# Optimization experiments

Hardware: AMD Instinct MI355X
Metric: run time of the kernel (lower is better)

## Reference

```python
import jax, jax.numpy as jnp
import numpy as np

D_MODEL = 512
N_HEADS = 8
D_K = 64
D_V = 64
FACTOR = 1  # Autoformer AutoCorrelation default


def setup_inputs() -> dict:
    key = jax.random.key(0)
    ks = jax.random.split(key, 7)
    B, L = 8, 2048
    Q = jax.random.normal(ks[0], (B, L, D_MODEL), dtype=jnp.float32)
    K = jax.random.normal(ks[1], (B, L, D_MODEL), dtype=jnp.float32)
    V = jax.random.normal(ks[2], (B, L, D_MODEL), dtype=jnp.float32)
    s = 1.0 / np.sqrt(D_MODEL)
    WQ = jax.random.normal(ks[3], (D_MODEL, N_HEADS * D_K), dtype=jnp.float32) * s
    WK = jax.random.normal(ks[4], (D_MODEL, N_HEADS * D_K), dtype=jnp.float32) * s
    WV = jax.random.normal(ks[5], (D_MODEL, N_HEADS * D_V), dtype=jnp.float32) * s
    Wfc = jax.random.normal(ks[6], (N_HEADS * D_V, D_MODEL), dtype=jnp.float32) * s
    return {"Q": Q, "K": K, "V": V, "WQ": WQ, "WK": WK, "WV": WV, "Wfc": Wfc}


def _autocorrelation(q, k, v):
    # q, k, v: [B, L, H, E] (Autoformer AutoCorrelation, training-mode agg)
    B, L, H, E = q.shape
    qf = jnp.fft.rfft(q.transpose(0, 2, 3, 1), axis=-1)  # [B,H,E,Lf]
    kf = jnp.fft.rfft(k.transpose(0, 2, 3, 1), axis=-1)
    corr = jnp.fft.irfft(qf * jnp.conj(kf), n=L, axis=-1)  # [B,H,E,L]
    vals = v.transpose(0, 2, 3, 1)  # [B,H,E,L]
    top_k = int(FACTOR * np.log(L))
    mean_value = corr.mean(axis=(1, 2))  # [B,L] mean over heads & channels
    _, index = jax.lax.top_k(mean_value.mean(axis=0), top_k)  # [top_k] shared delays
    weights = mean_value[:, index]  # [B, top_k]
    tmp_corr = jax.nn.softmax(weights, axis=-1)  # [B, top_k]
    # roll(vals, -index[i]) along time for each selected delay, fully vectorized
    gather_idx = (jnp.arange(L)[None, :] + index[:, None]) % L  # [top_k, L]
    rolled = vals[..., gather_idx]  # [B,H,E,top_k,L]
    agg = jnp.einsum('bhekl,bk->bhel', rolled, tmp_corr)  # [B,H,E,L]
    return agg.transpose(0, 3, 1, 2)  # [B,L,H,E]


def reference(Q, K, V, WQ, WK, WV, Wfc):
    B, L, _ = Q.shape
    q_s = (Q @ WQ).reshape(B, L, N_HEADS, D_K)
    k_s = (K @ WK).reshape(B, L, N_HEADS, D_K)
    v_s = (V @ WV).reshape(B, L, N_HEADS, D_V)
    context = _autocorrelation(q_s, k_s, v_s)  # [B,L,H,Dv]
    context = context.reshape(B, L, N_HEADS * D_V)
    return context @ Wfc  # [B,L,d_model]
```

## Files before the change

### kernel.cpp

```cpp
#include <hip/hip_runtime.h>
#include <math.h>

#define B_ 8
#define L_ 2048
#define D_ 512
#define LOG2L 11
#define TOPK 7
#define M_ (B_ * L_)

typedef __attribute__((ext_vector_type(8))) _Float16 half8;
typedef __attribute__((ext_vector_type(4))) _Float16 half4;
typedef __attribute__((ext_vector_type(4))) float f32x4;

__global__ __launch_bounds__(256) void convw_kernel(
    const float* __restrict__ W0, const float* __restrict__ W1,
    const float* __restrict__ W2, const float* __restrict__ W3,
    _Float16* __restrict__ T0, _Float16* __restrict__ T1,
    _Float16* __restrict__ T2, _Float16* __restrict__ T3)
{
  __shared__ float tile[64][65];
  const int t = (int)threadIdx.x;
  const int mat = (int)blockIdx.x >> 6;
  const int tb = (int)blockIdx.x & 63;
  const float* W = (mat == 0) ? W0 : (mat == 1) ? W1 : (mat == 2) ? W2 : W3;
  _Float16* Wt = (mat == 0) ? T0 : (mat == 1) ? T1 : (mat == 2) ? T2 : T3;
  const int k0 = (tb >> 3) * 64;
  const int n0 = (tb & 7) * 64;
#pragma unroll
  for (int i = 0; i < 4; ++i) {
    const int kl = (t >> 4) + i * 16;
    const float4 v = *reinterpret_cast<const float4*>(&W[(size_t)(k0 + kl) * D_ + n0 + (t & 15) * 4]);
    tile[kl][(t & 15) * 4 + 0] = v.x;
    tile[kl][(t & 15) * 4 + 1] = v.y;
    tile[kl][(t & 15) * 4 + 2] = v.z;
    tile[kl][(t & 15) * 4 + 3] = v.w;
  }
  __syncthreads();
  const int nl = t >> 2, q = t & 3;
  half8 h0, h1;
#pragma unroll
  for (int j = 0; j < 8; ++j) {
    h0[j] = (_Float16)tile[q * 16 + j][nl];
    h1[j] = (_Float16)tile[q * 16 + 8 + j][nl];
  }
  _Float16* dst = &Wt[(size_t)(n0 + nl) * D_ + k0 + q * 16];
  *reinterpret_cast<half8*>(dst) = h0;
  *reinterpret_cast<half8*>(dst + 8) = h1;
}

#define LDSTR 40

template <int INBF, int OUTMODE>
__global__ __launch_bounds__(256) void gemm_f16_kernel(
    const float* __restrict__ Af, const _Float16* __restrict__ Ah,
    const _Float16* __restrict__ Wt,
    float* __restrict__ Cf, _Float16* __restrict__ Ch)
{
  __shared__ __align__(16) char smem[128 * LDSTR * 2 * 2];
  _Float16* sA = (_Float16*)smem;
  _Float16* sB = sA + 128 * LDSTR;

  const int tid = (int)threadIdx.x;
  const int lane = tid & 63, wave = tid >> 6;
  const int wr = (wave >> 1) << 6, wc = (wave & 1) << 6;
  const int m0 = ((int)blockIdx.x >> 2) << 7;
  const int n0 = ((int)blockIdx.x & 3) << 7;

  const int srow = tid >> 1;
  const int sc0 = (tid & 1) << 4;

  f32x4 acc[4][4];
  const f32x4 zero = {0.f, 0.f, 0.f, 0.f};
#pragma unroll
  for (int i = 0; i < 4; ++i)
#pragma unroll
    for (int j = 0; j < 4; ++j) acc[i][j] = zero;

  const int fr = lane & 15;
  const int g8 = (lane >> 4) << 3;

  for (int k0 = 0; k0 < D_; k0 += 32) {
    half8 ha0, ha1, hb0, hb1;
    if constexpr (INBF == 0) {
      const float* ap = Af + (size_t)(m0 + srow) * D_ + k0 + sc0;
      float tmp[16];
#pragma unroll
      for (int j = 0; j < 4; ++j) {
        const float4 v = *reinterpret_cast<const float4*>(ap + j * 4);
        tmp[j * 4 + 0] = v.x; tmp[j * 4 + 1] = v.y;
        tmp[j * 4 + 2] = v.z; tmp[j * 4 + 3] = v.w;
      }
#pragma unroll
      for (int j = 0; j < 8; ++j) { ha0[j] = (_Float16)tmp[j]; ha1[j] = (_Float16)tmp[8 + j]; }
    } else {
      const _Float16* ap = Ah + (size_t)(m0 + srow) * D_ + k0 + sc0;
      ha0 = *reinterpret_cast<const half8*>(ap);
      ha1 = *reinterpret_cast<const half8*>(ap + 8);
    }
    {
      const _Float16* bp = Wt + (size_t)(n0 + srow) * D_ + k0 + sc0;
      hb0 = *reinterpret_cast<const half8*>(bp);
      hb1 = *reinterpret_cast<const half8*>(bp + 8);
    }

    __syncthreads();
    *reinterpret_cast<half8*>(&sA[srow * LDSTR + sc0]) = ha0;
    *reinterpret_cast<half8*>(&sA[srow * LDSTR + sc0 + 8]) = ha1;
    *reinterpret_cast<half8*>(&sB[srow * LDSTR + sc0]) = hb0;
    *reinterpret_cast<half8*>(&sB[srow * LDSTR + sc0 + 8]) = hb1;
    __syncthreads();

    half8 afr[4], bfr[4];
#pragma unroll
    for (int i = 0; i < 4; ++i) {
      afr[i] = *reinterpret_cast<const half8*>(&sA[(wr + i * 16 + fr) * LDSTR + g8]);
      bfr[i] = *reinterpret_cast<const half8*>(&sB[(wc + i * 16 + fr) * LDSTR + g8]);
    }
#pragma unroll
    for (int mi = 0; mi < 4; ++mi)
#pragma unroll
      for (int ni = 0; ni < 4; ++ni)
        acc[mi][ni] = __builtin_amdgcn_mfma_f32_16x16x32_f16(afr[mi], bfr[ni], acc[mi][ni], 0, 0, 0);
  }

  const int orow = (lane >> 4) << 2;
  const int ocol = lane & 15;
  if constexpr (OUTMODE == 0) {
#pragma unroll
    for (int mi = 0; mi < 4; ++mi)
#pragma unroll
      for (int ni = 0; ni < 4; ++ni)
#pragma unroll
        for (int r = 0; r < 4; ++r)
          Cf[(size_t)(m0 + wr + mi * 16 + orow + r) * D_ + n0 + wc + ni * 16 + ocol] = acc[mi][ni][r];
  } else if constexpr (OUTMODE == 2) {
#pragma unroll
    for (int mi = 0; mi < 4; ++mi)
#pragma unroll
      for (int ni = 0; ni < 4; ++ni)
#pragma unroll
        for (int r = 0; r < 4; ++r)
          Ch[(size_t)(m0 + wr + mi * 16 + orow + r) * D_ + n0 + wc + ni * 16 + ocol] = (_Float16)acc[mi][ni][r];
  } else {
#pragma unroll
    for (int ni = 0; ni < 4; ++ni) {
      const size_t nrow = (size_t)(n0 + wc + ni * 16 + ocol) * M_;
#pragma unroll
      for (int mi = 0; mi < 4; ++mi) {
        half4 hv;
        hv[0] = (_Float16)acc[mi][ni][0]; hv[1] = (_Float16)acc[mi][ni][1];
        hv[2] = (_Float16)acc[mi][ni][2]; hv[3] = (_Float16)acc[mi][ni][3];
        *reinterpret_cast<half4*>(&Ch[nrow + m0 + wr + mi * 16 + orow]) = hv;
      }
    }
  }
}

__device__ __forceinline__ int rev11(int x) {
  return (int)(__brev((unsigned)x) >> (32 - LOG2L));
}

#define DCHUNK 4
#define PADI(i) ((i) + ((i) >> 5))

#define BFLY(j0, j1, wr_, wi_) { \
  const float ar = xr[j0], ai = xi[j0], br = xr[j1], bi = xi[j1]; \
  xr[j0] = ar + br; xi[j0] = ai + bi; \
  const float tr = ar - br, ti = ai - bi; \
  xr[j1] = tr * (wr_) - ti * (wi_); \
  xi[j1] = tr * (wi_) + ti * (wr_); }

__global__ __launch_bounds__(256) void corr_fft_kernel(
    const _Float16* __restrict__ qT, const _Float16* __restrict__ kT,
    float* __restrict__ S)
{
  __shared__ float re[2112];
  __shared__ float im[2112];
  const int t = (int)threadIdx.x;
  const int blk = (int)blockIdx.x;
  const int b = blk >> 7;
  const int d0 = (blk & 127) * DCHUNK;
  const int u2 = t & 31, u3 = t & 3;

  float w2048r, w2048i, w256r, w256i, w32r, w32i;
  {
    float s_, c_;
    __sincosf(-6.283185307179586f * (float)t / 2048.f, &s_, &c_);
    w2048r = c_; w2048i = s_;
    __sincosf(-6.283185307179586f * (float)u2 / 256.f, &s_, &c_);
    w256r = c_; w256i = s_;
    __sincosf(-6.283185307179586f * (float)u3 / 32.f, &s_, &c_);
    w32r = c_; w32i = s_;
  }
  const float w1024r = w2048r * w2048r - w2048i * w2048i, w1024i = 2.f * w2048r * w2048i;
  const float w512r  = w1024r * w1024r - w1024i * w1024i, w512i  = 2.f * w1024r * w1024i;
  const float w128r  = w256r * w256r - w256i * w256i,     w128i  = 2.f * w256r * w256i;
  const float w64r   = w128r * w128r - w128i * w128i,     w64i   = 2.f * w128r * w128i;
  const float w16r   = w32r * w32r - w32i * w32i,         w16i   = 2.f * w32r * w32i;
  const float w8r    = w16r * w16r - w16i * w16i,         w8i    = 2.f * w16r * w16i;

  const float C_ = 0.70710678118654752f;
  const float W8R[4] = {1.f, C_, 0.f, -C_};
  const float W8I[4] = {0.f, -C_, -1.f, -C_};

  float pr[8] = {}, pi_[8] = {};

  for (int dc = 0; dc < DCHUNK; ++dc) {
    const int d = d0 + dc;
    const _Float16* qrow = qT + (size_t)d * M_ + (size_t)b * L_;
    const _Float16* krow = kT + (size_t)d * M_ + (size_t)b * L_;

    float xr[8], xi[8];
#pragma unroll
    for (int j = 0; j < 8; ++j) {
      xr[j] = (float)qrow[t + 256 * j];
      xi[j] = (float)krow[t + 256 * j];
    }

#pragma unroll
    for (int j = 0; j < 4; ++j) {
      const float wr_ = w2048r * W8R[j] - w2048i * W8I[j];
      const float wi_ = w2048r * W8I[j] + w2048i * W8R[j];
      BFLY(j, j + 4, wr_, wi_);
    }
#pragma unroll
    for (int base = 0; base < 8; base += 4) {
      BFLY(base + 0, base + 2, w1024r, w1024i);
      BFLY(base + 1, base + 3, w1024i, -w1024r);
    }
#pragma unroll
    for (int a = 0; a < 8; a += 2) BFLY(a, a + 1, w512r, w512i);

    __syncthreads();
#pragma unroll
    for (int j = 0; j < 8; ++j) {
      const int p = t + 256 * j;
      re[PADI(p)] = xr[j]; im[PADI(p)] = xi[j];
    }
    __syncthreads();
#pragma unroll
    for (int j = 0; j < 8; ++j) {
      const int p = ((t >> 5) << 8) + u2 + 32 * j;
      xr[j] = re[PADI(p)]; xi[j] = im[PADI(p)];
    }

#pragma unroll
    for (int j = 0; j < 4; ++j) {
      const float wr_ = w256r * W8R[j] - w256i * W8I[j];
      const float wi_ = w256r * W8I[j] + w256i * W8R[j];
      BFLY(j, j + 4, wr_, wi_);
    }
#pragma unroll
    for (int base = 0; base < 8; base += 4) {
      BFLY(base + 0, base + 2, w128r, w128i);
      BFLY(base + 1, base + 3, w128i, -w128r);
    }
#pragma unroll
    for (int a = 0; a < 8; a += 2) BFLY(a, a + 1, w64r, w64i);

    __syncthreads();
#pragma unroll
    for (int j = 0; j < 8; ++j) {
      const int p = ((t >> 5) << 8) + u2 + 32 * j;
      re[PADI(p)] = xr[j]; im[PADI(p)] = xi[j];
    }
    __syncthreads();
#pragma unroll
    for (int j = 0; j < 8; ++j) {
      const int p = ((t >> 2) << 5) + u3 + 4 * j;
      xr[j] = re[PADI(p)]; xi[j] = im[PADI(p)];
    }

#pragma unroll
    for (int j = 0; j < 4; ++j) {
      const float wr_ = w32r * W8R[j] - w32i * W8I[j];
      const float wi_ = w32r * W8I[j] + w32i * W8R[j];
      BFLY(j, j + 4, wr_, wi_);
    }
#pragma unroll
    for (int base = 0; base < 8; base += 4) {
      BFLY(base + 0, base + 2, w16r, w16i);
      BFLY(base + 1, base + 3, w16i, -w16r);
    }
#pragma unroll
    for (int a = 0; a < 8; a += 2) BFLY(a, a + 1, w8r, w8i);

    __syncthreads();
#pragma unroll
    for (int j = 0; j < 8; ++j) {
      const int p = ((t >> 2) << 5) + u3 + 4 * j;
      re[PADI(p)] = xr[j]; im[PADI(p)] = xi[j];
    }
    __syncthreads();
#pragma unroll
    for (int j = 0; j < 8; ++j) {
      const int p = 8 * t + j;
      xr[j] = re[PADI(p)]; xi[j] = im[PADI(p)];
    }

#pragma unroll
    for (int base = 0; base < 8; base += 4) {
      BFLY(base + 0, base + 2, 1.f, 0.f);
      BFLY(base + 1, base + 3, 0.f, -1.f);
    }
#pragma unroll
    for (int a = 0; a < 8; a += 2) BFLY(a, a + 1, 1.f, 0.f);

#pragma unroll
    for (int j = 0; j < 8; ++j) {
      const int p = 8 * t + j;
      re[PADI(p)] = xr[j]; im[PADI(p)] = xi[j];
    }
    __syncthreads();

#pragma unroll
    for (int i = 0; i < 8; ++i) {
      const int p = t + 256 * i;
      const int f = rev11(p);
      const int fm = (L_ - f) & (L_ - 1);
      const int pm = rev11(fm);
      const float Ar = re[PADI(p)],  Ai = im[PADI(p)];
      const float Br = re[PADI(pm)], Bi = -im[PADI(pm)];
      const float Qr = 0.5f * (Ar + Br), Qi = 0.5f * (Ai + Bi);
      const float Cr = 0.5f * (Ai - Bi), Ci = 0.5f * (Ar - Br);
      pr[i]  += Qr * Cr - Qi * Ci;
      pi_[i] += Qr * Ci + Qi * Cr;
    }
  }

#pragma unroll
  for (int i = 0; i < 8; ++i) {
    const int p = t + 256 * i;
    atomicAdd(&S[((size_t)b * L_ + p) * 2 + 0], pr[i]);
    atomicAdd(&S[((size_t)b * L_ + p) * 2 + 1], pi_[i]);
  }
}

__global__ __launch_bounds__(256) void ifft_kernel(
    const float* __restrict__ S, float* __restrict__ mv)
{
  __shared__ float re[L_];
  __shared__ float im[L_];
  const int b = blockIdx.x;
  for (int p = (int)threadIdx.x; p < L_; p += 256) {
    re[p] = S[((size_t)b * L_ + p) * 2 + 0];
    im[p] = S[((size_t)b * L_ + p) * 2 + 1];
  }
  __syncthreads();
  for (int s = 1; s <= LOG2L; ++s) {
    const int half = 1 << (s - 1);
    for (int j = (int)threadIdx.x; j < (L_ >> 1); j += 256) {
      const int pos = j & (half - 1);
      const int i0 = ((j >> (s - 1)) << s) + pos;
      const int i1 = i0 + half;
      const float ang = 3.14159265358979323846f * (float)pos / (float)half;
      float wi, wr;
      __sincosf(ang, &wi, &wr);
      const float br = re[i1], bi = im[i1];
      const float tr = br * wr - bi * wi;
      const float ti = br * wi + bi * wr;
      const float ar = re[i0], ai = im[i0];
      re[i0] = ar + tr; im[i0] = ai + ti;
      re[i1] = ar - tr; im[i1] = ai - ti;
    }
    __syncthreads();
  }
  const float scale = 1.0f / ((float)D_ * (float)L_);
  for (int l = (int)threadIdx.x; l < L_; l += 256)
    mv[(size_t)b * L_ + l] = re[l] * scale;
}

__global__ __launch_bounds__(1024) void topk_kernel(
    const float* __restrict__ mv, int* __restrict__ idx, float* __restrict__ wts)
{
  __shared__ float vals[L_];
  __shared__ float wm[16];
  __shared__ int wi[16];
  __shared__ int chosen[TOPK];
  const int t = (int)threadIdx.x;
  const int lane = t & 63, wv = t >> 6;
  float s0 = 0.f, s1 = 0.f;
#pragma unroll
  for (int b = 0; b < B_; ++b) {
    s0 += mv[(size_t)b * L_ + t];
    s1 += mv[(size_t)b * L_ + t + 1024];
  }
  vals[t] = s0; vals[t + 1024] = s1;
  __syncthreads();
  for (int kk = 0; kk < TOPK; ++kk) {
    float v0 = vals[t]; int i0 = t;
    const float v1 = vals[t + 1024];
    if (v1 > v0) { v0 = v1; i0 = t + 1024; }
#pragma unroll
    for (int off = 32; off; off >>= 1) {
      const float ov = __shfl_xor(v0, off, 64);
      const int oi = __shfl_xor(i0, off, 64);
      if (ov > v0 || (ov == v0 && oi < i0)) { v0 = ov; i0 = oi; }
    }
    if (lane == 0) { wm[wv] = v0; wi[wv] = i0; }
    __syncthreads();
    if (t == 0) {
      float m = wm[0]; int mi = wi[0];
      for (int i2 = 1; i2 < 16; ++i2)
        if (wm[i2] > m || (wm[i2] == m && wi[i2] < mi)) { m = wm[i2]; mi = wi[i2]; }
      chosen[kk] = mi; idx[kk] = mi; vals[mi] = -1e30f;
    }
    __syncthreads();
  }
  if (t < B_) {
    float w[TOPK];
    float mx = -1e30f;
#pragma unroll
    for (int kk = 0; kk < TOPK; ++kk) {
      w[kk] = mv[(size_t)t * L_ + chosen[kk]];
      mx = fmaxf(mx, w[kk]);
    }
    float sum = 0.f;
#pragma unroll
    for (int kk = 0; kk < TOPK; ++kk) { w[kk] = __expf(w[kk] - mx); sum += w[kk]; }
    const float inv = 1.0f / sum;
#pragma unroll
    for (int kk = 0; kk < TOPK; ++kk) wts[t * TOPK + kk] = w[kk] * inv;
  }
}

__global__ __launch_bounds__(128) void context_kernel(
    const _Float16* __restrict__ v, const int* __restrict__ idx,
    const float* __restrict__ wts, _Float16* __restrict__ ctx)
{
  const int bl = (int)blockIdx.x;
  const int b = bl >> LOG2L;
  const int l = bl & (L_ - 1);
  const int c = (int)threadIdx.x;
  float acc0 = 0.f, acc1 = 0.f, acc2 = 0.f, acc3 = 0.f;
#pragma unroll
  for (int kk = 0; kk < TOPK; ++kk) {
    const float w = wts[b * TOPK + kk];
    const int src = (l + idx[kk]) & (L_ - 1);
    const half4 x = *reinterpret_cast<const half4*>(v + ((size_t)(b << LOG2L) + src) * D_ + c * 4);
    acc0 = fmaf(w, (float)x[0], acc0);
    acc1 = fmaf(w, (float)x[1], acc1);
    acc2 = fmaf(w, (float)x[2], acc2);
    acc3 = fmaf(w, (float)x[3], acc3);
  }
  half4 o;
  o[0] = (_Float16)acc0; o[1] = (_Float16)acc1;
  o[2] = (_Float16)acc2; o[3] = (_Float16)acc3;
  *reinterpret_cast<half4*>(ctx + ((size_t)(b << LOG2L) + l) * D_ + c * 4) = o;
}

extern "C" void kernel_launch(void* const* d_in, const int* in_sizes, int n_in,
                              void* d_out, int out_size, void* d_ws, size_t ws_size,
                              hipStream_t stream)
{
  (void)in_sizes; (void)n_in; (void)out_size; (void)ws_size;
  const float* Q   = (const float*)d_in[0];
  const float* K   = (const float*)d_in[1];
  const float* V   = (const float*)d_in[2];
  const float* WQ  = (const float*)d_in[3];
  const float* WK  = (const float*)d_in[4];
  const float* WV  = (const float*)d_in[5];
  const float* Wfc = (const float*)d_in[6];
  float* out = (float*)d_out;

  char* ws = (char*)d_ws;
  const size_t sz_h   = (size_t)M_ * D_ * sizeof(_Float16);
  const size_t sz_w16 = (size_t)D_ * D_ * sizeof(_Float16);
  _Float16*  qT16  = (_Float16*)(ws);
  _Float16*  kT16  = (_Float16*)(ws + sz_h);
  _Float16*  vs16  = (_Float16*)(ws + 2 * sz_h);
  _Float16*  ctx16 = (_Float16*)(ws + 3 * sz_h);
  _Float16*  WQt   = (_Float16*)(ws + 4 * sz_h);
  _Float16*  WKt   = (_Float16*)(ws + 4 * sz_h + sz_w16);
  _Float16*  WVt   = (_Float16*)(ws + 4 * sz_h + 2 * sz_w16);
  _Float16*  Wfct  = (_Float16*)(ws + 4 * sz_h + 3 * sz_w16);
  float*     S     = (float*)(ws + 4 * sz_h + 4 * sz_w16);
  float*     mv    = (float*)((char*)S + (size_t)B_ * L_ * 2 * sizeof(float));
  int*       idx   = (int*)((char*)mv + (size_t)B_ * L_ * sizeof(float));
  float*     wts   = (float*)((char*)idx + 64);

  convw_kernel<<<256, 256, 0, stream>>>(WQ, WK, WV, Wfc, WQt, WKt, WVt, Wfct);

  gemm_f16_kernel<0, 3><<<512, 256, 0, stream>>>(Q, nullptr, WQt, nullptr, qT16);
  gemm_f16_kernel<0, 3><<<512, 256, 0, stream>>>(K, nullptr, WKt, nullptr, kT16);

  hipMemsetAsync(S, 0, (size_t)B_ * L_ * 2 * sizeof(float), stream);
  corr_fft_kernel<<<B_ * (D_ / DCHUNK), 256, 0, stream>>>(qT16, kT16, S);
  ifft_kernel<<<B_, 256, 0, stream>>>(S, mv);
  topk_kernel<<<1, 1024, 0, stream>>>(mv, idx, wts);

  gemm_f16_kernel<0, 2><<<512, 256, 0, stream>>>(V, nullptr, WVt, nullptr, vs16);
  context_kernel<<<B_ * L_, 128, 0, stream>>>(vs16, idx, wts, ctx16);
  gemm_f16_kernel<1, 0><<<512, 256, 0, stream>>>(nullptr, ctx16, Wfct, out, nullptr);
}
```

Before: 182.5 us.

## Batch QKV GEMMs, halve FFT chunk, use Hermitian symmetry, widen context loads

Merges the three Q/K/V projection GEMMs into one 1536-block launch, with the output mode chosen at runtime. Halves DCHUNK so the correlation FFT kernel launches twice as many blocks, adding a sync between chunks. Atomic accumulation now covers only the non-redundant half of the spectrum, and the inverse FFT rebuilds the rest from conjugate symmetry. The context kernel processes four rows per 256-thread block with half8 loads. The runtime output-mode branch and the smaller per-block FFT work may add overhead in exchange for fewer launches and less atomic traffic.

```diff
diff --git a/kernel.cpp b/kernel.cpp
--- a/kernel.cpp
+++ b/kernel.cpp
@@ -50,11 +50,12 @@
 
 #define LDSTR 40
 
-template <int INBF, int OUTMODE>
-__global__ __launch_bounds__(256) void gemm_f16_kernel(
+template <int INBF>
+__device__ __forceinline__ void gemm_body(
     const float* __restrict__ Af, const _Float16* __restrict__ Ah,
     const _Float16* __restrict__ Wt,
-    float* __restrict__ Cf, _Float16* __restrict__ Ch)
+    float* __restrict__ Cf, _Float16* __restrict__ Ch,
+    int outmode, int blk)
 {
   __shared__ __align__(16) char smem[128 * LDSTR * 2 * 2];
   _Float16* sA = (_Float16*)smem;
@@ -63,8 +64,8 @@
   const int tid = (int)threadIdx.x;
   const int lane = tid & 63, wave = tid >> 6;
   const int wr = (wave >> 1) << 6, wc = (wave & 1) << 6;
-  const int m0 = ((int)blockIdx.x >> 2) << 7;
-  const int n0 = ((int)blockIdx.x & 3) << 7;
+  const int m0 = (blk >> 2) << 7;
+  const int n0 = (blk & 3) << 7;
 
   const int srow = tid >> 1;
   const int sc0 = (tid & 1) << 4;
@@ -125,7 +126,7 @@
 
   const int orow = (lane >> 4) << 2;
   const int ocol = lane & 15;
-  if constexpr (OUTMODE == 0) {
+  if (outmode == 0) {
 #pragma unroll
     for (int mi = 0; mi < 4; ++mi)
 #pragma unroll
@@ -133,7 +134,7 @@
 #pragma unroll
         for (int r = 0; r < 4; ++r)
           Cf[(size_t)(m0 + wr + mi * 16 + orow + r) * D_ + n0 + wc + ni * 16 + ocol] = acc[mi][ni][r];
-  } else if constexpr (OUTMODE == 2) {
+  } else if (outmode == 2) {
 #pragma unroll
     for (int mi = 0; mi < 4; ++mi)
 #pragma unroll
@@ -156,11 +157,34 @@
   }
 }
 
+__global__ __launch_bounds__(256) void gemm_qkv_kernel(
+    const float* __restrict__ Q, const float* __restrict__ K,
+    const float* __restrict__ V,
+    const _Float16* __restrict__ WQt, const _Float16* __restrict__ WKt,
+    const _Float16* __restrict__ WVt,
+    _Float16* __restrict__ qT16, _Float16* __restrict__ kT16,
+    _Float16* __restrict__ vs16)
+{
+  const int mat = (int)blockIdx.x >> 9;
+  const int blk = (int)blockIdx.x & 511;
+  const float* A = (mat == 0) ? Q : (mat == 1) ? K : V;
+  const _Float16* Wt = (mat == 0) ? WQt : (mat == 1) ? WKt : WVt;
+  _Float16* Ch = (mat == 0) ? qT16 : (mat == 1) ? kT16 : vs16;
+  gemm_body<0>(A, nullptr, Wt, nullptr, Ch, (mat == 2) ? 2 : 3, blk);
+}
+
+__global__ __launch_bounds__(256) void gemm_fc_kernel(
+    const _Float16* __restrict__ ctx16, const _Float16* __restrict__ Wfct,
+    float* __restrict__ out)
+{
+  gemm_body<1>(nullptr, ctx16, Wfct, out, nullptr, 0, (int)blockIdx.x);
+}
+
 __device__ __forceinline__ int rev11(int x) {
   return (int)(__brev((unsigned)x) >> (32 - LOG2L));
 }
 
-#define DCHUNK 4
+#define DCHUNK 2
 #define PADI(i) ((i) + ((i) >> 5))
 
 #define BFLY(j0, j1, wr_, wi_) { \
@@ -178,8 +202,8 @@
   __shared__ float im[2112];
   const int t = (int)threadIdx.x;
   const int blk = (int)blockIdx.x;
-  const int b = blk >> 7;
-  const int d0 = (blk & 127) * DCHUNK;
+  const int b = blk >> 8;
+  const int d0 = (blk & 255) * DCHUNK;
   const int u2 = t & 31, u3 = t & 3;
 
   float w2048r, w2048i, w256r, w256i, w32r, w32i;
@@ -326,13 +350,17 @@
       pr[i]  += Qr * Cr - Qi * Ci;
       pi_[i] += Qr * Ci + Qi * Cr;
     }
+    if (dc + 1 < DCHUNK) __syncthreads();
   }
 
 #pragma unroll
   for (int i = 0; i < 8; ++i) {
     const int p = t + 256 * i;
-    atomicAdd(&S[((size_t)b * L_ + p) * 2 + 0], pr[i]);
-    atomicAdd(&S[((size_t)b * L_ + p) * 2 + 1], pi_[i]);
+    const int f = rev11(p);
+    if (f <= L_ / 2) {
+      atomicAdd(&S[((size_t)b * L_ + p) * 2 + 0], pr[i]);
+      atomicAdd(&S[((size_t)b * L_ + p) * 2 + 1], pi_[i]);
+    }
   }
 }
 
@@ -343,8 +371,17 @@
   __shared__ float im[L_];
   const int b = blockIdx.x;
   for (int p = (int)threadIdx.x; p < L_; p += 256) {
-    re[p] = S[((size_t)b * L_ + p) * 2 + 0];
-    im[p] = S[((size_t)b * L_ + p) * 2 + 1];
+    const int f = rev11(p);
+    float sr, si;
+    if (f <= L_ / 2) {
+      sr = S[((size_t)b * L_ + p) * 2 + 0];
+      si = S[((size_t)b * L_ + p) * 2 + 1];
+    } else {
+      const int pm = rev11(L_ - f);
+      sr = S[((size_t)b * L_ + pm) * 2 + 0];
+      si = -S[((size_t)b * L_ + pm) * 2 + 1];
+    }
+    re[p] = sr; im[p] = si;
   }
   __syncthreads();
   for (int s = 1; s <= LOG2L; ++s) {
@@ -424,29 +461,27 @@
   }
 }
 
-__global__ __launch_bounds__(128) void context_kernel(
+__global__ __launch_bounds__(256) void context_kernel(
     const _Float16* __restrict__ v, const int* __restrict__ idx,
     const float* __restrict__ wts, _Float16* __restrict__ ctx)
 {
-  const int bl = (int)blockIdx.x;
-  const int b = bl >> LOG2L;
-  const int l = bl & (L_ - 1);
-  const int c = (int)threadIdx.x;
-  float acc0 = 0.f, acc1 = 0.f, acc2 = 0.f, acc3 = 0.f;
+  const int blk = (int)blockIdx.x;
+  const int b = blk >> 9;
+  const int l = ((blk & 511) << 2) + ((int)threadIdx.x >> 6);
+  const int lane = (int)threadIdx.x & 63;
+  float acc[8] = {};
 #pragma unroll
   for (int kk = 0; kk < TOPK; ++kk) {
     const float w = wts[b * TOPK + kk];
     const int src = (l + idx[kk]) & (L_ - 1);
-    const half4 x = *reinterpret_cast<const half4*>(v + ((size_t)(b << LOG2L) + src) * D_ + c * 4);
-    acc0 = fmaf(w, (float)x[0], acc0);
-    acc1 = fmaf(w, (float)x[1], acc1);
-    acc2 = fmaf(w, (float)x[2], acc2);
-    acc3 = fmaf(w, (float)x[3], acc3);
-  }
-  half4 o;
-  o[0] = (_Float16)acc0; o[1] = (_Float16)acc1;
-  o[2] = (_Float16)acc2; o[3] = (_Float16)acc3;
-  *reinterpret_cast<half4*>(ctx + ((size_t)(b << LOG2L) + l) * D_ + c * 4) = o;
+    const half8 x = *reinterpret_cast<const half8*>(v + ((size_t)(b << LOG2L) + src) * D_ + lane * 8);
+#pragma unroll
+    for (int j = 0; j < 8; ++j) acc[j] = fmaf(w, (float)x[j], acc[j]);
+  }
+  half8 o;
+#pragma unroll
+  for (int j = 0; j < 8; ++j) o[j] = (_Float16)acc[j];
+  *reinterpret_cast<half8*>(ctx + ((size_t)(b << LOG2L) + l) * D_ + lane * 8) = o;
 }
 
 extern "C" void kernel_launch(void* const* d_in, const int* in_sizes, int n_in,
@@ -480,16 +515,14 @@
   float*     wts   = (float*)((char*)idx + 64);
 
   convw_kernel<<<256, 256, 0, stream>>>(WQ, WK, WV, Wfc, WQt, WKt, WVt, Wfct);
-
-  gemm_f16_kernel<0, 3><<<512, 256, 0, stream>>>(Q, nullptr, WQt, nullptr, qT16);
-  gemm_f16_kernel<0, 3><<<512, 256, 0, stream>>>(K, nullptr, WKt, nullptr, kT16);
-
   hipMemsetAsync(S, 0, (size_t)B_ * L_ * 2 * sizeof(float), stream);
+
+  gemm_qkv_kernel<<<1536, 256, 0, stream>>>(Q, K, V, WQt, WKt, WVt, qT16, kT16, vs16);
+
   corr_fft_kernel<<<B_ * (D_ / DCHUNK), 256, 0, stream>>>(qT16, kT16, S);
   ifft_kernel<<<B_, 256, 0, stream>>>(S, mv);
   topk_kernel<<<1, 1024, 0, stream>>>(mv, idx, wts);
 
-  gemm_f16_kernel<0, 2><<<512, 256, 0, stream>>>(V, nullptr, WVt, nullptr, vs16);
-  context_kernel<<<B_ * L_, 128, 0, stream>>>(vs16, idx, wts, ctx16);
-  gemm_f16_kernel<1, 0><<<512, 256, 0, stream>>>(nullptr, ctx16, Wfct, out, nullptr);
-}
+  context_kernel<<<4096, 256, 0, stream>>>(vs16, idx, wts, ctx16);
+  gemm_fc_kernel<<<512, 256, 0, stream>>>(ctx16, Wfct, out);
+}
```

Result: slower. 214.8 us (+17.7%).
